# Kernel optimization log

Measured on AMD Instinct MI355X. Metric: run time of the kernel, lower is better.

Reference implementation:

```python
import jax, jax.numpy as jnp
from jax import lax
import numpy as np

D_MODEL = 512
D_STATE = 16
D_CONV = 4
EXPAND = 2
D_INNER = EXPAND * D_MODEL
DT_RANK = (D_MODEL + 15) // 16  # ceil(d_model/16) = 32
B, L = 4, 1024


def setup_inputs() -> dict:
    key = jax.random.key(0)
    ks = jax.random.split(key, 12)
    s = 0.02
    inp = {
        "feature": jax.random.normal(ks[0], (B, L, D_MODEL), jnp.float32),
        "ln_w": jnp.ones((D_MODEL,), jnp.float32),
        "ln_b": jnp.zeros((D_MODEL,), jnp.float32),
        "in_proj_w": jax.random.normal(ks[1], (2 * D_INNER, D_MODEL), jnp.float32) * s,
        "conv_w": jax.random.normal(ks[2], (D_INNER, D_CONV), jnp.float32) * 0.1,
        "conv_b": jnp.zeros((D_INNER,), jnp.float32),
        "x_proj_w": jax.random.normal(ks[3], (DT_RANK + 2 * D_STATE, D_INNER), jnp.float32) * s,
        "dt_proj_w": jax.random.normal(ks[4], (D_INNER, DT_RANK), jnp.float32) * 0.1,
        "dt_proj_b": jax.random.normal(ks[5], (D_INNER,), jnp.float32) * 0.1 - 4.0,
        "A_log": jnp.log(jnp.broadcast_to(jnp.arange(1, D_STATE + 1, dtype=jnp.float32), (D_INNER, D_STATE))),
        "D": jnp.ones((D_INNER,), jnp.float32),
        "out_proj_w": jax.random.normal(ks[6], (D_MODEL, D_INNER), jnp.float32) * s,
    }
    return inp


def _mamba_block(xn, in_proj_w, conv_w, conv_b, x_proj_w, dt_proj_w, dt_proj_b, A_log, D, out_proj_w):
    # xn: [B, L, d_model]
    xz = jnp.einsum('bld,ed->ble', xn, in_proj_w)          # [B, L, 2*d_inner]
    x, z = xz[..., :D_INNER], xz[..., D_INNER:]
    # causal depthwise conv along L
    xc = jnp.transpose(x, (0, 2, 1))                        # [B, d_inner, L]
    xc = lax.conv_general_dilated(
        xc, conv_w[:, None, :], (1,), [(D_CONV - 1, 0)],
        feature_group_count=D_INNER,
        dimension_numbers=('NCH', 'OIH', 'NCH')) + conv_b[None, :, None]
    x = jax.nn.silu(jnp.transpose(xc, (0, 2, 1)))           # [B, L, d_inner]
    x_dbl = jnp.einsum('bld,ed->ble', x, x_proj_w)          # [B, L, dt_rank+2*d_state]
    dt = x_dbl[..., :DT_RANK]
    Bm = x_dbl[..., DT_RANK:DT_RANK + D_STATE]
    Cm = x_dbl[..., DT_RANK + D_STATE:]
    dt = jax.nn.softplus(jnp.einsum('blr,dr->bld', dt, dt_proj_w) + dt_proj_b)  # [B,L,d_inner]
    A = -jnp.exp(A_log)                                     # [d_inner, d_state]

    def step(h, inp):
        dt_t, B_t, C_t, x_t = inp                           # [B,d_inner],[B,d_state],[B,d_state],[B,d_inner]
        dA = jnp.exp(dt_t[..., None] * A)                   # [B, d_inner, d_state]
        h = dA * h + (dt_t * x_t)[..., None] * B_t[:, None, :]
        y = jnp.einsum('bds,bs->bd', h, C_t)
        return h, y

    xs = (jnp.transpose(dt, (1, 0, 2)), jnp.transpose(Bm, (1, 0, 2)),
          jnp.transpose(Cm, (1, 0, 2)), jnp.transpose(x, (1, 0, 2)))
    h0 = jnp.zeros((xn.shape[0], D_INNER, D_STATE), xn.dtype)
    _, ys = lax.scan(step, h0, xs)                          # ys: [L, B, d_inner]
    y = jnp.transpose(ys, (1, 0, 2)) + x * D
    y = y * jax.nn.silu(z)
    return jnp.einsum('bld,ed->ble', y, out_proj_w)         # [B, L, d_model]


def reference(feature, ln_w, ln_b, in_proj_w, conv_w, conv_b, x_proj_w,
              dt_proj_w, dt_proj_b, A_log, D, out_proj_w):
    eps = 1e-5
    mu = jnp.mean(feature, axis=-1, keepdims=True)
    var = jnp.var(feature, axis=-1, keepdims=True)
    xn = (feature - mu) / jnp.sqrt(var + eps) * ln_w + ln_b
    out = _mamba_block(xn, in_proj_w, conv_w, conv_b, x_proj_w,
                       dt_proj_w, dt_proj_b, A_log, D, out_proj_w)
    return xn + out
```

## Files before the change

### kernel.cpp

```cpp
#include <hip/hip_runtime.h>
#include <hip/hip_bf16.h>
#include <math.h>

#define B_SZ 4
#define L_SZ 1024
#define DM   512
#define DI   1024
#define DS   16
#define DTR  32
#define NXD  64
#define M_ROWS (B_SZ*L_SZ)
#define CHK  32
#define CLEN 32
#define NCH  (B_SZ*DI)
#define PLANE (NCH*DS)
#define LDA  40

typedef __attribute__((ext_vector_type(8))) short short8;
typedef __attribute__((ext_vector_type(4))) float f32x4;
typedef __hip_bfloat16 bf16;

__device__ __forceinline__ float bf2f(bf16 x){ return __bfloat162float(x); }
__device__ __forceinline__ float fsig(float x){ return __builtin_amdgcn_rcpf(1.f + __expf(-x)); }
__device__ __forceinline__ unsigned short bfbits(float x){ bf16 b = __float2bfloat16(x); return *(unsigned short*)&b; }
#define LOG2E 1.44269504f

__device__ __forceinline__ bool is_f32(const void* lnw){
    return *(const unsigned*)lnw == 0x3F800000u;
}
__device__ __forceinline__ float loadf(const void* s, int i, bool f){
    return f ? ((const float*)s)[i] : bf2f(((const bf16*)s)[i]);
}
__device__ __forceinline__ bf16 loadb(const void* s, int i, bool f){
    return f ? __float2bfloat16(((const float*)s)[i]) : ((const bf16*)s)[i];
}

#define CVT_TOTAL 1694720
__global__ __launch_bounds__(256) void prep_kernel(
        const void* __restrict__ feat, const void* __restrict__ lnw, const void* __restrict__ lnb,
        const void* __restrict__ w_in, const void* __restrict__ w_x, const void* __restrict__ w_out,
        const void* __restrict__ w_dt, const void* __restrict__ b_dt,
        const void* __restrict__ alog, const void* __restrict__ dvec,
        const void* __restrict__ cw, const void* __restrict__ cb,
        bf16* __restrict__ WINB, bf16* __restrict__ WXB, bf16* __restrict__ WOUTB,
        float* __restrict__ WDTT, float* __restrict__ BDT, float* __restrict__ ALOG,
        float* __restrict__ DVEC, float* __restrict__ CWF, float* __restrict__ CBF,
        float* __restrict__ xn, bf16* __restrict__ xnb, float* __restrict__ XDBL) {
    bool f = is_f32(lnw);
    if (blockIdx.y == 0) {
        int id = blockIdx.x*256 + threadIdx.x;
        if (id < M_ROWS*NXD) XDBL[id] = 0.f;
        #pragma unroll 2
        for (int g = id; g < CVT_TOTAL; g += 1048576) {
            if      (g < 1048576)  WINB[g] = loadb(w_in, g, f);
            else if (g < 1114112)  WXB[g-1048576] = loadb(w_x, g-1048576, f);
            else if (g < 1638400)  WOUTB[g-1114112] = loadb(w_out, g-1114112, f);
            else if (g < 1671168){ int i = g-1638400; WDTT[(i&(DTR-1))*DI + (i>>5)] = loadf(w_dt, i, f); }
            else if (g < 1672192)  BDT[g-1671168] = loadf(b_dt, g-1671168, f);
            else if (g < 1688576)  ALOG[g-1672192] = loadf(alog, g-1672192, f);
            else if (g < 1689600)  DVEC[g-1688576] = loadf(dvec, g-1688576, f);
            else if (g < 1693696)  CWF[g-1689600] = loadf(cw, g-1689600, f);
            else                   CBF[g-1693696] = loadf(cb, g-1693696, f);
        }
    } else {
        int row = blockIdx.x;
        int t = threadIdx.x;
        size_t base = (size_t)row*DM;
        float v0 = loadf(feat, base+t, f);
        float v1 = loadf(feat, base+t+256, f);
        __shared__ float ssum[256], ssq[256];
        ssum[t] = v0+v1; ssq[t] = v0*v0+v1*v1;
        __syncthreads();
        for (int off=128; off>0; off>>=1){
            if (t<off){ ssum[t]+=ssum[t+off]; ssq[t]+=ssq[t+off]; }
            __syncthreads();
        }
        float mu  = ssum[0]*(1.0f/DM);
        float var = ssq[0]*(1.0f/DM) - mu*mu;
        float rstd = rsqrtf(var + 1e-5f);
        float o0 = (v0-mu)*rstd*loadf(lnw,t,f)     + loadf(lnb,t,f);
        float o1 = (v1-mu)*rstd*loadf(lnw,t+256,f) + loadf(lnb,t+256,f);
        xn[base + t]      = o0;
        xn[base + t+256]  = o1;
        xnb[base + t]     = __float2bfloat16(o0);
        xnb[base + t+256] = __float2bfloat16(o1);
    }
}


__global__ __launch_bounds__(256) void gemm_in_mfma(const bf16* __restrict__ A,
        const bf16* __restrict__ W, bf16* __restrict__ XB, bf16* __restrict__ ZB) {
    const int K = 512;
    __shared__ bf16 As[128*LDA];
    __shared__ bf16 Bs[128*LDA];
    int t = threadIdx.x;
    int w = t>>6, l = t&63;
    int wm = w&1, wn = w>>1;
    int row0 = blockIdx.y*128, col0 = blockIdx.x*128;
    int lr = l&15, lq = l>>4;
    int srow = t>>2, scol = (t&3)*8;
    const bf16* pA0 = A + (size_t)(row0+srow)*K    + scol;
    const bf16* pA1 = A + (size_t)(row0+64+srow)*K + scol;
    const bf16* pB0 = W + (size_t)(col0+srow)*K    + scol;
    const bf16* pB1 = W + (size_t)(col0+64+srow)*K + scol;
    f32x4 acc[4][4] = {};
    short8 a0 = *(const short8*)(pA0);
    short8 a1 = *(const short8*)(pA1);
    short8 b0 = *(const short8*)(pB0);
    short8 b1 = *(const short8*)(pB1);
    for (int k0=0; k0<K; k0+=32) {
        __syncthreads();
        *(short8*)(As + srow*LDA + scol)      = a0;
        *(short8*)(As + (64+srow)*LDA + scol) = a1;
        *(short8*)(Bs + srow*LDA + scol)      = b0;
        *(short8*)(Bs + (64+srow)*LDA + scol) = b1;
        __syncthreads();
        if (k0 + 32 < K) {
            a0 = *(const short8*)(pA0 + k0 + 32);
            a1 = *(const short8*)(pA1 + k0 + 32);
            b0 = *(const short8*)(pB0 + k0 + 32);
            b1 = *(const short8*)(pB1 + k0 + 32);
        }
        short8 af[4], bfr[4];
        #pragma unroll
        for (int mi=0;mi<4;mi++) af[mi]  = *(const short8*)(As + (wm*64+mi*16+lr)*LDA + lq*8);
        #pragma unroll
        for (int ni=0;ni<4;ni++) bfr[ni] = *(const short8*)(Bs + (wn*64+ni*16+lr)*LDA + lq*8);
        #pragma unroll
        for (int mi=0;mi<4;mi++)
            #pragma unroll
            for (int ni=0;ni<4;ni++)
                acc[mi][ni] = __builtin_amdgcn_mfma_f32_16x16x32_bf16(af[mi], bfr[ni], acc[mi][ni], 0,0,0);
    }
    bf16* dst; int cbn;
    if (col0 < DI) { dst = XB; cbn = col0; } else { dst = ZB; cbn = col0 - DI; }
    #pragma unroll
    for (int mi=0;mi<4;mi++)
        #pragma unroll
        for (int ni=0;ni<4;ni++) {
            int r = row0 + wm*64 + mi*16 + lq*4;
            int c = cbn  + wn*64 + ni*16 + lr;
            #pragma unroll
            for (int rr=0;rr<4;rr++)
                dst[(size_t)(r+rr)*DI + c] = __float2bfloat16(acc[mi][ni][rr]);
        }
}

__global__ __launch_bounds__(256) void gemm_xc_mfma(const bf16* __restrict__ XB,
        const bf16* __restrict__ W, const float* __restrict__ cw, const float* __restrict__ cb,
        bf16* __restrict__ XC, float* __restrict__ C) {
    const int K = 1024;
    __shared__ bf16 As[64*LDA];
    __shared__ bf16 Bs[64*LDA];
    int t = threadIdx.x;
    int w = t>>6, l64 = t&63;
    int wm = w&1, wn = w>>1;
    int row0 = blockIdx.y*64;
    int kbeg = blockIdx.x*(K/4), kend = kbeg + K/4;
    int lr = l64&15, lq = l64>>4;
    int srow = t>>2, scol = (t&3)*8;
    int m = row0 + srow;
    int lpos = m & (L_SZ-1);
    bool vr0 = lpos >= 3, vr1 = lpos >= 2, vr2 = lpos >= 1;
    const bf16* pxb = XB + (size_t)(m-3)*DI + kbeg + scol;
    const bf16* pB0 = W + (size_t)srow*K + kbeg + scol;
    f32x4 acc[2][2] = {};
    short8 x0 = *(const short8*)(pxb);
    short8 x1 = *(const short8*)(pxb + DI);
    short8 x2 = *(const short8*)(pxb + 2*DI);
    short8 x3 = *(const short8*)(pxb + 3*DI);
    short8 b0 = *(const short8*)(pB0);
    for (int k0=kbeg; k0<kend; k0+=32) {
        int dbase = k0 + scol;
        short8 xx0 = x0, xx1 = x1, xx2 = x2;
        if (!vr0) xx0 = (short8){0,0,0,0,0,0,0,0};
        if (!vr1) xx1 = (short8){0,0,0,0,0,0,0,0};
        if (!vr2) xx2 = (short8){0,0,0,0,0,0,0,0};
        uint a0[4], a1[4], a2[4], a3[4];
        *(uint4*)a0 = *(uint4*)&xx0; *(uint4*)a1 = *(uint4*)&xx1;
        *(uint4*)a2 = *(uint4*)&xx2; *(uint4*)a3 = *(uint4*)&x3;
        uint outw[4];
        #pragma unroll
        for (int jw=0; jw<4; jw++){
            float r2[2];
            #pragma unroll
            for (int hi=0; hi<2; hi++){
                int dch = dbase + jw*2 + hi;
                float4 wv = *(const float4*)(cw + (size_t)dch*4);
                float accv = cb[dch];
                float e0 = hi ? __uint_as_float(a0[jw] & 0xffff0000u) : __uint_as_float(a0[jw] << 16);
                float e1 = hi ? __uint_as_float(a1[jw] & 0xffff0000u) : __uint_as_float(a1[jw] << 16);
                float e2 = hi ? __uint_as_float(a2[jw] & 0xffff0000u) : __uint_as_float(a2[jw] << 16);
                float e3 = hi ? __uint_as_float(a3[jw] & 0xffff0000u) : __uint_as_float(a3[jw] << 16);
                accv = fmaf(e0, wv.x, accv); accv = fmaf(e1, wv.y, accv);
                accv = fmaf(e2, wv.z, accv); accv = fmaf(e3, wv.w, accv);
                r2[hi] = accv * fsig(accv);
            }
            outw[jw] = (uint)bfbits(r2[0]) | ((uint)bfbits(r2[1]) << 16);
        }
        short8 cv; *(uint4*)&cv = *(uint4*)outw;
        __syncthreads();
        *(short8*)(As + srow*LDA + scol) = cv;
        *(short8*)(Bs + srow*LDA + scol) = b0;
        __syncthreads();
        *(short8*)(XC + (size_t)m*DI + dbase) = cv;
        if (k0 + 32 < kend) {
            pxb += 32; pB0 += 32;
            x0 = *(const short8*)(pxb);
            x1 = *(const short8*)(pxb + DI);
            x2 = *(const short8*)(pxb + 2*DI);
            x3 = *(const short8*)(pxb + 3*DI);
            b0 = *(const short8*)(pB0);
        }
        short8 af[2], bfr[2];
        #pragma unroll
        for (int mi=0;mi<2;mi++) af[mi]  = *(const short8*)(As + (wm*32+mi*16+lr)*LDA + lq*8);
        #pragma unroll
        for (int ni=0;ni<2;ni++) bfr[ni] = *(const short8*)(Bs + (wn*32+ni*16+lr)*LDA + lq*8);
        #pragma unroll
        for (int mi=0;mi<2;mi++)
            #pragma unroll
            for (int ni=0;ni<2;ni++)
                acc[mi][ni] = __builtin_amdgcn_mfma_f32_16x16x32_bf16(af[mi], bfr[ni], acc[mi][ni], 0,0,0);
    }
    #pragma unroll
    for (int mi=0;mi<2;mi++)
        #pragma unroll
        for (int ni=0;ni<2;ni++) {
            int r = row0 + wm*32 + mi*16 + lq*4;
            int c = wn*32 + ni*16 + lr;
            #pragma unroll
            for (int rr=0;rr<4;rr++)
                atomicAdd(&C[(size_t)(r+rr)*NXD + c], acc[mi][ni][rr]);
        }
}

__global__ __launch_bounds__(256) void gemm_out_mfma(const bf16* __restrict__ A,
        const bf16* __restrict__ W, const float* __restrict__ xn,
        void* __restrict__ out, const void* __restrict__ lnw) {
    const int K = 1024;
    __shared__ bf16 As[128*LDA];
    __shared__ bf16 Bs[128*LDA];
    int t = threadIdx.x;
    int w = t>>6, l = t&63;
    int wm = w&1, wn = w>>1;
    int row0 = blockIdx.y*128, col0 = blockIdx.x*128;
    int lr = l&15, lq = l>>4;
    int srow = t>>2, scol = (t&3)*8;
    const bf16* pA0 = A + (size_t)(row0+srow)*K    + scol;
    const bf16* pA1 = A + (size_t)(row0+64+srow)*K + scol;
    const bf16* pB0 = W + (size_t)(col0+srow)*K    + scol;
    const bf16* pB1 = W + (size_t)(col0+64+srow)*K + scol;
    f32x4 acc[4][4] = {};
    short8 a0 = *(const short8*)(pA0);
    short8 a1 = *(const short8*)(pA1);
    short8 b0 = *(const short8*)(pB0);
    short8 b1 = *(const short8*)(pB1);
    for (int k0=0; k0<K; k0+=32) {
        __syncthreads();
        *(short8*)(As + srow*LDA + scol)      = a0;
        *(short8*)(As + (64+srow)*LDA + scol) = a1;
        *(short8*)(Bs + srow*LDA + scol)      = b0;
        *(short8*)(Bs + (64+srow)*LDA + scol) = b1;
        __syncthreads();
        if (k0 + 32 < K) {
            a0 = *(const short8*)(pA0 + k0 + 32);
            a1 = *(const short8*)(pA1 + k0 + 32);
            b0 = *(const short8*)(pB0 + k0 + 32);
            b1 = *(const short8*)(pB1 + k0 + 32);
        }
        short8 af[4], bfr[4];
        #pragma unroll
        for (int mi=0;mi<4;mi++) af[mi]  = *(const short8*)(As + (wm*64+mi*16+lr)*LDA + lq*8);
        #pragma unroll
        for (int ni=0;ni<4;ni++) bfr[ni] = *(const short8*)(Bs + (wn*64+ni*16+lr)*LDA + lq*8);
        #pragma unroll
        for (int mi=0;mi<4;mi++)
            #pragma unroll
            for (int ni=0;ni<4;ni++)
                acc[mi][ni] = __builtin_amdgcn_mfma_f32_16x16x32_bf16(af[mi], bfr[ni], acc[mi][ni], 0,0,0);
    }
    bool f = is_f32(lnw);
    #pragma unroll
    for (int mi=0;mi<4;mi++)
        #pragma unroll
        for (int ni=0;ni<4;ni++) {
            int r = row0 + wm*64 + mi*16 + lq*4;
            int c = col0 + wn*64 + ni*16 + lr;
            #pragma unroll
            for (int rr=0;rr<4;rr++) {
                float v = acc[mi][ni][rr] + xn[(size_t)(r+rr)*DM + c];
                if (f) ((float*)out)[(size_t)(r+rr)*DM + c] = v;
                else   ((bf16*)out)[(size_t)(r+rr)*DM + c] = __float2bfloat16(v);
            }
        }
}

__global__ __launch_bounds__(256) void dt_kernel(const float* __restrict__ xdbl,
        const float* __restrict__ dtwT, const float* __restrict__ dtb,
        bf16* __restrict__ dtf) {
    int m0 = blockIdx.x*4;
    int d0 = threadIdx.x*4;
    float4 bias = *(const float4*)(dtb + d0);
    float4 a0 = bias, a1 = bias, a2 = bias, a3 = bias;
    const float* xr = xdbl + (size_t)m0*NXD;
    #pragma unroll 4
    for (int r=0; r<DTR; r++) {
        float4 wv = *(const float4*)(dtwT + r*DI + d0);
        float x0 = xr[r], x1 = xr[NXD+r], x2 = xr[2*NXD+r], x3 = xr[3*NXD+r];
        a0.x = fmaf(wv.x,x0,a0.x); a0.y = fmaf(wv.y,x0,a0.y); a0.z = fmaf(wv.z,x0,a0.z); a0.w = fmaf(wv.w,x0,a0.w);
        a1.x = fmaf(wv.x,x1,a1.x); a1.y = fmaf(wv.y,x1,a1.y); a1.z = fmaf(wv.z,x1,a1.z); a1.w = fmaf(wv.w,x1,a1.w);
        a2.x = fmaf(wv.x,x2,a2.x); a2.y = fmaf(wv.y,x2,a2.y); a2.z = fmaf(wv.z,x2,a2.z); a2.w = fmaf(wv.w,x2,a2.w);
        a3.x = fmaf(wv.x,x3,a3.x); a3.y = fmaf(wv.y,x3,a3.y); a3.z = fmaf(wv.z,x3,a3.z); a3.w = fmaf(wv.w,x3,a3.w);
    }
    float4 accs[4] = {a0, a1, a2, a3};
    #pragma unroll
    for (int mm=0; mm<4; mm++) {
        float4 v = accs[mm];
        v.x = (v.x > 20.f) ? v.x : __logf(1.f + __expf(v.x));
        v.y = (v.y > 20.f) ? v.y : __logf(1.f + __expf(v.y));
        v.z = (v.z > 20.f) ? v.z : __logf(1.f + __expf(v.z));
        v.w = (v.w > 20.f) ? v.w : __logf(1.f + __expf(v.w));
        uint2 pk;
        pk.x = (unsigned)bfbits(v.x) | ((unsigned)bfbits(v.y) << 16);
        pk.y = (unsigned)bfbits(v.z) | ((unsigned)bfbits(v.w) << 16);
        *(uint2*)(dtf + (size_t)(m0+mm)*DI + d0) = pk;
    }
}


__global__ __launch_bounds__(256) void scan_p1(const bf16* __restrict__ dtf,
        const bf16* __restrict__ xc, const float* __restrict__ xdbl,
        const float* __restrict__ A_log, float* __restrict__ SP, float* __restrict__ PP) {
    int ch = blockIdx.x*256 + threadIdx.x;
    int j  = blockIdx.y;
    int d  = ch & (DI-1);
    int bu = __builtin_amdgcn_readfirstlane(ch >> 10);
    float a2[DS];
    {
        const float4* pa = (const float4*)(A_log + d*DS);
        #pragma unroll
        for (int q=0;q<4;q++){
            float4 v = pa[q];
            a2[q*4+0] = -__expf(v.x)*LOG2E; a2[q*4+1] = -__expf(v.y)*LOG2E;
            a2[q*4+2] = -__expf(v.z)*LOG2E; a2[q*4+3] = -__expf(v.w)*LOG2E;
        }
    }
    float h[DS], P[DS];
    #pragma unroll
    for (int s=0;s<DS;s++){ h[s]=0.f; P[s]=1.f; }
    size_t row = (size_t)bu*L_SZ + (size_t)j*CLEN;
    const bf16* pdt = dtf + row*DI + d;
    const bf16* pxc = xc  + row*DI + d;
    const float* pB = xdbl + row*NXD + DTR;
    #pragma unroll 2
    for (int t=0; t<CLEN; t++) {
        float dt = bf2f(*pdt);
        float u  = dt * bf2f(*pxc);
        #pragma unroll
        for (int s=0;s<DS;s++){
            float dA = __builtin_exp2f(dt*a2[s]);
            h[s] = fmaf(dA, h[s], u*pB[s]);
            P[s] *= dA;
        }
        pdt += DI; pxc += DI; pB += NXD;
    }
    float* sp = SP + (size_t)j*PLANE + ch;
    float* pp = PP + (size_t)j*PLANE + ch;
    #pragma unroll
    for (int s=0;s<DS;s++){ sp[s*NCH] = h[s]; pp[s*NCH] = P[s]; }
}

__global__ void scan_p2(const float* __restrict__ SP, const float* __restrict__ PP,
                        float* __restrict__ HB) {
    int idx = blockIdx.x*256 + threadIdx.x;
    float H = 0.f;
    for (int j=0;j<CHK;j++){
        size_t o = (size_t)j*PLANE + idx;
        float p = PP[o], s = SP[o];
        HB[o] = H;
        H = fmaf(p, H, s);
    }
}

__global__ __launch_bounds__(256) void scan_p3(const bf16* __restrict__ dtf,
        const bf16* __restrict__ xc, const float* __restrict__ xdbl,
        const float* __restrict__ A_log, const float* __restrict__ Dp,
        const float* __restrict__ HB, const bf16* __restrict__ zb,
        bf16* __restrict__ ybf) {
    int ch = blockIdx.x*256 + threadIdx.x;
    int j  = blockIdx.y;
    int d  = ch & (DI-1);
    int bu = __builtin_amdgcn_readfirstlane(ch >> 10);
    float a2[DS];
    {
        const float4* pa = (const float4*)(A_log + d*DS);
        #pragma unroll
        for (int q=0;q<4;q++){
            float4 v = pa[q];
            a2[q*4+0] = -__expf(v.x)*LOG2E; a2[q*4+1] = -__expf(v.y)*LOG2E;
            a2[q*4+2] = -__expf(v.z)*LOG2E; a2[q*4+3] = -__expf(v.w)*LOG2E;
        }
    }
    float h[DS];
    {
        const float* ph = HB + (size_t)j*PLANE + ch;
        #pragma unroll
        for (int s=0;s<DS;s++) h[s] = ph[s*NCH];
    }
    float Dd = Dp[d];
    size_t row = (size_t)bu*L_SZ + (size_t)j*CLEN;
    const bf16* pdt = dtf + row*DI + d;
    const bf16* pxc = xc  + row*DI + d;
    const float* pB = xdbl + row*NXD + DTR;
    const float* pC = pB + DS;
    const bf16* pz  = zb  + row*DI + d;
    bf16*       py  = ybf + row*DI + d;
    #pragma unroll 2
    for (int t=0; t<CLEN; t++) {
        float dt = bf2f(*pdt);
        float xv = bf2f(*pxc);
        float u  = dt * xv;
        float y0=0.f, y1=0.f, y2=0.f, y3=0.f;
        #pragma unroll
        for (int s=0;s<DS;s+=4){
            float dA0 = __builtin_exp2f(dt*a2[s]);
            float dA1 = __builtin_exp2f(dt*a2[s+1]);
            float dA2 = __builtin_exp2f(dt*a2[s+2]);
            float dA3 = __builtin_exp2f(dt*a2[s+3]);
            h[s]   = fmaf(dA0, h[s],   u*pB[s]);
            h[s+1] = fmaf(dA1, h[s+1], u*pB[s+1]);
            h[s+2] = fmaf(dA2, h[s+2], u*pB[s+2]);
            h[s+3] = fmaf(dA3, h[s+3], u*pB[s+3]);
            y0 = fmaf(h[s],   pC[s],   y0);
            y1 = fmaf(h[s+1], pC[s+1], y1);
            y2 = fmaf(h[s+2], pC[s+2], y2);
            y3 = fmaf(h[s+3], pC[s+3], y3);
        }
        float y = (y0+y1) + (y2+y3) + xv*Dd;
        float z = bf2f(*pz);
        *py = __float2bfloat16(y * z * fsig(z));
        pdt += DI; pxc += DI; pB += NXD; pC += NXD; pz += DI; py += DI;
    }
}

extern "C" void kernel_launch(void* const* d_in, const int* in_sizes, int n_in,
                              void* d_out, int out_size, void* d_ws, size_t ws_size,
                              hipStream_t stream) {
    float* FW = (float*)d_ws;
    float* SP   = FW;
    float* PP   = FW + 2097152;
    float* HB   = FW + 4194304;
    bf16*  XNB  = (bf16*)(FW + 4194304);
    float* XN   = FW + 6291456;
    bf16*  DTF  = (bf16*)(FW + 8388608);
    float* XDBL = FW + 12582912;
    float* WDTT = FW + 12851200;
    float* BDT  = FW + 12883968;
    float* ALOG = FW + 12884992;
    float* DVEC = FW + 12901376;
    float* CWF  = FW + 12902400;
    float* CBF  = FW + 12906496;
    bf16* XBB  = (bf16*)(FW + 12907520);
    bf16* YBF  = XBB;
    bf16* ZBB  = (bf16*)(FW + 15004672);
    bf16* XCB  = (bf16*)(FW + 17101824);
    bf16* WINB = (bf16*)(FW + 19198976);
    bf16* WXB  = (bf16*)(FW + 19723264);
    bf16* WOUTB= (bf16*)(FW + 19756032);

    prep_kernel<<<dim3(4096, 2), 256, 0, stream>>>(
        d_in[0], d_in[1], d_in[2], d_in[3], d_in[6], d_in[11], d_in[7], d_in[8],
        d_in[9], d_in[10], d_in[4], d_in[5],
        WINB, WXB, WOUTB, WDTT, BDT, ALOG, DVEC, CWF, CBF, XN, XNB, XDBL);
    gemm_in_mfma<<<dim3(2048/128, M_ROWS/128), 256, 0, stream>>>(XNB, WINB, XBB, ZBB);
    gemm_xc_mfma<<<dim3(4, M_ROWS/64), 256, 0, stream>>>(XBB, WXB, CWF, CBF, XCB, XDBL);
    dt_kernel<<<M_ROWS/4, 256, 0, stream>>>(XDBL, WDTT, BDT, DTF);
    scan_p1<<<dim3(NCH/256, CHK), 256, 0, stream>>>(DTF, XCB, XDBL, ALOG, SP, PP);
    scan_p2<<<PLANE/256, 256, 0, stream>>>(SP, PP, HB);
    scan_p3<<<dim3(NCH/256, CHK), 256, 0, stream>>>(DTF, XCB, XDBL, ALOG, DVEC, HB, ZBB, YBF);
    gemm_out_mfma<<<dim3(DM/128, M_ROWS/128), 256, 0, stream>>>(YBF, WOUTB, XN, d_out, d_in[1]);
}
```

Measured before the change: 231.2 us.

## Fuse dt projection and softplus into scan kernels; drop fp32 xn buffer

Removes the separate dt_kernel and recomputes the dt projection (32-wide dot product plus softplus) inline in both scan_p1 and scan_p3. Each thread keeps its 32 dt weights in registers and reads x_dbl rows directly, so the bf16 dt tensor is never written or read. The fp32 layernorm output is also dropped, and the residual add in the output GEMM reads the bf16 copy instead, cutting memory traffic. In exchange the scans do the dt matmul twice and use more registers, and the residual loses precision by going through bf16.

```diff
diff --git a/kernel.cpp b/kernel.cpp
--- a/kernel.cpp
+++ b/kernel.cpp
@@ -45,7 +45,7 @@
         bf16* __restrict__ WINB, bf16* __restrict__ WXB, bf16* __restrict__ WOUTB,
         float* __restrict__ WDTT, float* __restrict__ BDT, float* __restrict__ ALOG,
         float* __restrict__ DVEC, float* __restrict__ CWF, float* __restrict__ CBF,
-        float* __restrict__ xn, bf16* __restrict__ xnb, float* __restrict__ XDBL) {
+        bf16* __restrict__ xnb, float* __restrict__ XDBL) {
     bool f = is_f32(lnw);
     if (blockIdx.y == 0) {
         int id = blockIdx.x*256 + threadIdx.x;
@@ -80,8 +80,6 @@
         float rstd = rsqrtf(var + 1e-5f);
         float o0 = (v0-mu)*rstd*loadf(lnw,t,f)     + loadf(lnb,t,f);
         float o1 = (v1-mu)*rstd*loadf(lnw,t+256,f) + loadf(lnb,t+256,f);
-        xn[base + t]      = o0;
-        xn[base + t+256]  = o1;
         xnb[base + t]     = __float2bfloat16(o0);
         xnb[base + t+256] = __float2bfloat16(o1);
     }
@@ -236,7 +234,7 @@
 }
 
 __global__ __launch_bounds__(256) void gemm_out_mfma(const bf16* __restrict__ A,
-        const bf16* __restrict__ W, const float* __restrict__ xn,
+        const bf16* __restrict__ W, const bf16* __restrict__ xnb,
         void* __restrict__ out, const void* __restrict__ lnw) {
     const int K = 1024;
     __shared__ bf16 As[128*LDA];
@@ -289,49 +287,18 @@
             int c = col0 + wn*64 + ni*16 + lr;
             #pragma unroll
             for (int rr=0;rr<4;rr++) {
-                float v = acc[mi][ni][rr] + xn[(size_t)(r+rr)*DM + c];
+                float v = acc[mi][ni][rr] + bf2f(xnb[(size_t)(r+rr)*DM + c]);
                 if (f) ((float*)out)[(size_t)(r+rr)*DM + c] = v;
                 else   ((bf16*)out)[(size_t)(r+rr)*DM + c] = __float2bfloat16(v);
             }
         }
 }
 
-__global__ __launch_bounds__(256) void dt_kernel(const float* __restrict__ xdbl,
-        const float* __restrict__ dtwT, const float* __restrict__ dtb,
-        bf16* __restrict__ dtf) {
-    int m0 = blockIdx.x*4;
-    int d0 = threadIdx.x*4;
-    float4 bias = *(const float4*)(dtb + d0);
-    float4 a0 = bias, a1 = bias, a2 = bias, a3 = bias;
-    const float* xr = xdbl + (size_t)m0*NXD;
-    #pragma unroll 4
-    for (int r=0; r<DTR; r++) {
-        float4 wv = *(const float4*)(dtwT + r*DI + d0);
-        float x0 = xr[r], x1 = xr[NXD+r], x2 = xr[2*NXD+r], x3 = xr[3*NXD+r];
-        a0.x = fmaf(wv.x,x0,a0.x); a0.y = fmaf(wv.y,x0,a0.y); a0.z = fmaf(wv.z,x0,a0.z); a0.w = fmaf(wv.w,x0,a0.w);
-        a1.x = fmaf(wv.x,x1,a1.x); a1.y = fmaf(wv.y,x1,a1.y); a1.z = fmaf(wv.z,x1,a1.z); a1.w = fmaf(wv.w,x1,a1.w);
-        a2.x = fmaf(wv.x,x2,a2.x); a2.y = fmaf(wv.y,x2,a2.y); a2.z = fmaf(wv.z,x2,a2.z); a2.w = fmaf(wv.w,x2,a2.w);
-        a3.x = fmaf(wv.x,x3,a3.x); a3.y = fmaf(wv.y,x3,a3.y); a3.z = fmaf(wv.z,x3,a3.z); a3.w = fmaf(wv.w,x3,a3.w);
-    }
-    float4 accs[4] = {a0, a1, a2, a3};
-    #pragma unroll
-    for (int mm=0; mm<4; mm++) {
-        float4 v = accs[mm];
-        v.x = (v.x > 20.f) ? v.x : __logf(1.f + __expf(v.x));
-        v.y = (v.y > 20.f) ? v.y : __logf(1.f + __expf(v.y));
-        v.z = (v.z > 20.f) ? v.z : __logf(1.f + __expf(v.z));
-        v.w = (v.w > 20.f) ? v.w : __logf(1.f + __expf(v.w));
-        uint2 pk;
-        pk.x = (unsigned)bfbits(v.x) | ((unsigned)bfbits(v.y) << 16);
-        pk.y = (unsigned)bfbits(v.z) | ((unsigned)bfbits(v.w) << 16);
-        *(uint2*)(dtf + (size_t)(m0+mm)*DI + d0) = pk;
-    }
-}
-
-
-__global__ __launch_bounds__(256) void scan_p1(const bf16* __restrict__ dtf,
-        const bf16* __restrict__ xc, const float* __restrict__ xdbl,
-        const float* __restrict__ A_log, float* __restrict__ SP, float* __restrict__ PP) {
+
+__global__ __launch_bounds__(256) void scan_p1(const bf16* __restrict__ xc,
+        const float* __restrict__ xdbl, const float* __restrict__ dtwT,
+        const float* __restrict__ dtb, const float* __restrict__ A_log,
+        float* __restrict__ SP, float* __restrict__ PP) {
     int ch = blockIdx.x*256 + threadIdx.x;
     int j  = blockIdx.y;
     int d  = ch & (DI-1);
@@ -346,24 +313,31 @@
             a2[q*4+2] = -__expf(v.z)*LOG2E; a2[q*4+3] = -__expf(v.w)*LOG2E;
         }
     }
+    float wdt[DTR];
+    #pragma unroll
+    for (int r=0;r<DTR;r++) wdt[r] = dtwT[r*DI + d];
+    float bias = dtb[d];
     float h[DS], P[DS];
     #pragma unroll
     for (int s=0;s<DS;s++){ h[s]=0.f; P[s]=1.f; }
     size_t row = (size_t)bu*L_SZ + (size_t)j*CLEN;
-    const bf16* pdt = dtf + row*DI + d;
     const bf16* pxc = xc  + row*DI + d;
-    const float* pB = xdbl + row*NXD + DTR;
+    const float* pX = xdbl + row*NXD;
     #pragma unroll 2
     for (int t=0; t<CLEN; t++) {
-        float dt = bf2f(*pdt);
+        float acc = bias;
+        #pragma unroll
+        for (int r=0;r<DTR;r++) acc = fmaf(pX[r], wdt[r], acc);
+        float dt = (acc > 20.f) ? acc : __logf(1.f + __expf(acc));
         float u  = dt * bf2f(*pxc);
+        const float* pB = pX + DTR;
         #pragma unroll
         for (int s=0;s<DS;s++){
             float dA = __builtin_exp2f(dt*a2[s]);
             h[s] = fmaf(dA, h[s], u*pB[s]);
             P[s] *= dA;
         }
-        pdt += DI; pxc += DI; pB += NXD;
+        pxc += DI; pX += NXD;
     }
     float* sp = SP + (size_t)j*PLANE + ch;
     float* pp = PP + (size_t)j*PLANE + ch;
@@ -383,11 +357,11 @@
     }
 }
 
-__global__ __launch_bounds__(256) void scan_p3(const bf16* __restrict__ dtf,
-        const bf16* __restrict__ xc, const float* __restrict__ xdbl,
-        const float* __restrict__ A_log, const float* __restrict__ Dp,
-        const float* __restrict__ HB, const bf16* __restrict__ zb,
-        bf16* __restrict__ ybf) {
+__global__ __launch_bounds__(256) void scan_p3(const bf16* __restrict__ xc,
+        const float* __restrict__ xdbl, const float* __restrict__ dtwT,
+        const float* __restrict__ dtb, const float* __restrict__ A_log,
+        const float* __restrict__ Dp, const float* __restrict__ HB,
+        const bf16* __restrict__ zb, bf16* __restrict__ ybf) {
     int ch = blockIdx.x*256 + threadIdx.x;
     int j  = blockIdx.y;
     int d  = ch & (DI-1);
@@ -402,6 +376,10 @@
             a2[q*4+2] = -__expf(v.z)*LOG2E; a2[q*4+3] = -__expf(v.w)*LOG2E;
         }
     }
+    float wdt[DTR];
+    #pragma unroll
+    for (int r=0;r<DTR;r++) wdt[r] = dtwT[r*DI + d];
+    float bias = dtb[d];
     float h[DS];
     {
         const float* ph = HB + (size_t)j*PLANE + ch;
@@ -410,17 +388,20 @@
     }
     float Dd = Dp[d];
     size_t row = (size_t)bu*L_SZ + (size_t)j*CLEN;
-    const bf16* pdt = dtf + row*DI + d;
     const bf16* pxc = xc  + row*DI + d;
-    const float* pB = xdbl + row*NXD + DTR;
-    const float* pC = pB + DS;
+    const float* pX = xdbl + row*NXD;
     const bf16* pz  = zb  + row*DI + d;
     bf16*       py  = ybf + row*DI + d;
     #pragma unroll 2
     for (int t=0; t<CLEN; t++) {
-        float dt = bf2f(*pdt);
+        float acc = bias;
+        #pragma unroll
+        for (int r=0;r<DTR;r++) acc = fmaf(pX[r], wdt[r], acc);
+        float dt = (acc > 20.f) ? acc : __logf(1.f + __expf(acc));
         float xv = bf2f(*pxc);
         float u  = dt * xv;
+        const float* pB = pX + DTR;
+        const float* pC = pX + DTR + DS;
         float y0=0.f, y1=0.f, y2=0.f, y3=0.f;
         #pragma unroll
         for (int s=0;s<DS;s+=4){
@@ -440,7 +421,7 @@
         float y = (y0+y1) + (y2+y3) + xv*Dd;
         float z = bf2f(*pz);
         *py = __float2bfloat16(y * z * fsig(z));
-        pdt += DI; pxc += DI; pB += NXD; pC += NXD; pz += DI; py += DI;
+        pxc += DI; pX += NXD; pz += DI; py += DI;
     }
 }
 
@@ -451,33 +432,30 @@
     float* SP   = FW;
     float* PP   = FW + 2097152;
     float* HB   = FW + 4194304;
-    bf16*  XNB  = (bf16*)(FW + 4194304);
-    float* XN   = FW + 6291456;
-    bf16*  DTF  = (bf16*)(FW + 8388608);
-    float* XDBL = FW + 12582912;
-    float* WDTT = FW + 12851200;
-    float* BDT  = FW + 12883968;
-    float* ALOG = FW + 12884992;
-    float* DVEC = FW + 12901376;
-    float* CWF  = FW + 12902400;
-    float* CBF  = FW + 12906496;
-    bf16* XBB  = (bf16*)(FW + 12907520);
+    bf16*  XNB  = (bf16*)(FW + 6291456);
+    float* XDBL = FW + 7340032;
+    float* WDTT = FW + 7602176;
+    float* BDT  = FW + 7634944;
+    float* ALOG = FW + 7635968;
+    float* DVEC = FW + 7652352;
+    float* CWF  = FW + 7653376;
+    float* CBF  = FW + 7657472;
+    bf16* XBB  = (bf16*)(FW + 7658496);
     bf16* YBF  = XBB;
-    bf16* ZBB  = (bf16*)(FW + 15004672);
-    bf16* XCB  = (bf16*)(FW + 17101824);
-    bf16* WINB = (bf16*)(FW + 19198976);
-    bf16* WXB  = (bf16*)(FW + 19723264);
-    bf16* WOUTB= (bf16*)(FW + 19756032);
+    bf16* ZBB  = (bf16*)(FW + 9755648);
+    bf16* XCB  = (bf16*)(FW + 11852800);
+    bf16* WINB = (bf16*)(FW + 13949952);
+    bf16* WXB  = (bf16*)(FW + 14474240);
+    bf16* WOUTB= (bf16*)(FW + 14507008);
 
     prep_kernel<<<dim3(4096, 2), 256, 0, stream>>>(
         d_in[0], d_in[1], d_in[2], d_in[3], d_in[6], d_in[11], d_in[7], d_in[8],
         d_in[9], d_in[10], d_in[4], d_in[5],
-        WINB, WXB, WOUTB, WDTT, BDT, ALOG, DVEC, CWF, CBF, XN, XNB, XDBL);
+        WINB, WXB, WOUTB, WDTT, BDT, ALOG, DVEC, CWF, CBF, XNB, XDBL);
     gemm_in_mfma<<<dim3(2048/128, M_ROWS/128), 256, 0, stream>>>(XNB, WINB, XBB, ZBB);
     gemm_xc_mfma<<<dim3(4, M_ROWS/64), 256, 0, stream>>>(XBB, WXB, CWF, CBF, XCB, XDBL);
-    dt_kernel<<<M_ROWS/4, 256, 0, stream>>>(XDBL, WDTT, BDT, DTF);
-    scan_p1<<<dim3(NCH/256, CHK), 256, 0, stream>>>(DTF, XCB, XDBL, ALOG, SP, PP);
+    scan_p1<<<dim3(NCH/256, CHK), 256, 0, stream>>>(XCB, XDBL, WDTT, BDT, ALOG, SP, PP);
     scan_p2<<<PLANE/256, 256, 0, stream>>>(SP, PP, HB);
-    scan_p3<<<dim3(NCH/256, CHK), 256, 0, stream>>>(DTF, XCB, XDBL, ALOG, DVEC, HB, ZBB, YBF);
-    gemm_out_mfma<<<dim3(DM/128, M_ROWS/128), 256, 0, stream>>>(YBF, WOUTB, XN, d_out, d_in[1]);
-}
+    scan_p3<<<dim3(NCH/256, CHK), 256, 0, stream>>>(XCB, XDBL, WDTT, BDT, ALOG, DVEC, HB, ZBB, YBF);
+    gemm_out_mfma<<<dim3(DM/128, M_ROWS/128), 256, 0, stream>>>(YBF, WOUTB, XNB, d_out, d_in[1]);
+}
```

Result: faster. 224.7 us (-2.8%).
